# Optimization experiments

Measured on AMD Instinct MI355X. Metric: run time of the kernel, lower is better.

## Reference

```python
import jax, jax.numpy as jnp
import numpy as np

# Module hyper-params (from init_kwargs)
M = 41            # filter taps (odd)
OVERLAPS = 40     # even
STRIDES = 216
N_FFT = OVERLAPS + STRIDES   # 256
HOP = STRIDES                # strides > 0 -> hop = strides
PAD = M // 2


def setup_inputs() -> dict:
    key = jax.random.key(0)
    ks = jax.random.split(key, 5)
    B, Nmodes = 2, 2
    steps = 4628
    L = (steps - 1) * HOP + N_FFT  # 999688, frames tile the signal exactly
    x_real = jax.random.normal(ks[0], (B, L, Nmodes), jnp.float32)
    x_imag = jax.random.normal(ks[1], (B, L, Nmodes), jnp.float32)
    task_info = jax.random.uniform(ks[2], (B, 4), jnp.float32)  # col 0 = power (dBm)
    # SnseFilter learned complex taps (shared across polarizations, step=1, n_fwm=0)
    h_real = jax.random.normal(ks[3], (M,), jnp.float32) * 0.01
    h_imag = jax.random.normal(ks[4], (M,), jnp.float32) * 0.01
    return {"x_real": x_real, "x_imag": x_imag, "task_info": task_info,
            "h_real": h_real, "h_imag": h_imag}


def _corr1d(I, h):
    # I: [N, Lp] real, h: [M] real -> valid cross-correlation [N, Lp-M+1]
    out = jax.lax.conv_general_dilated(I[:, None, :], h.reshape(1, 1, M),
                                       window_strides=(1,), padding='VALID')
    return out[:, 0, :]


def reference(x_real, x_imag, task_info, h_real, h_imag):
    x = x_real + 1j * x_imag          # [B, L, Nmodes] complex64
    B, L, Nm = x.shape
    steps = (L - N_FFT) // HOP + 1

    # ---- STFT along dim=1 (frame + FFT, rectangular window, center=False) ----
    idx = HOP * jnp.arange(steps)[:, None] + jnp.arange(N_FFT)[None, :]  # [steps, n_fft]
    frames = x[:, idx, :]                      # [B, steps, n_fft, Nm]
    X = jnp.fft.fft(frames, axis=2)            # frequency-domain frames

    # ---- periodic padding along frequency axis + SnseFilter (per-tap nonlinear PBC) ----
    Xp = jnp.concatenate([X[:, :, -PAD:, :], X, X[:, :, :PAD, :]], axis=2)  # [B,steps,Lp,Nm]
    I = jnp.sum(Xp.real ** 2 + Xp.imag ** 2, axis=-1)   # total intensity over modes [B,steps,Lp]
    Lp = N_FFT + 2 * PAD
    Ic = I.reshape(B * steps, Lp)
    phi = (_corr1d(Ic, h_real) + 1j * _corr1d(Ic, h_imag)).reshape(B, steps, N_FFT)
    # launch power from task_info (col 0 in dBm), per mode
    P = (10.0 ** (task_info[:, 0] / 10.0) / Nm).astype(jnp.float32)  # [B]
    # first-order perturbation: E_out = E + j * P * (h * I) * E  (Manakov diagonal term)
    Y = X * (1.0 + 1j * P[:, None, None, None] * phi[..., None])

    # ---- ISTFT: ifft each frame + overlap-add with rectangular-window normalization ----
    yf = jnp.fft.ifft(Y, axis=2)               # [B, steps, n_fft, Nm]
    flat_idx = idx.reshape(-1)
    ola = jnp.zeros((B, L, Nm), yf.dtype).at[:, flat_idx, :].add(
        yf.reshape(B, steps * N_FFT, Nm))
    wsum = jnp.zeros((L,), jnp.float32).at[flat_idx].add(1.0)  # frame coverage count
    y = ola / wsum[None, :, None]

    out = y[:, OVERLAPS // 2: L - OVERLAPS // 2, :]   # [B, L-overlaps, Nm] complex
    return jnp.stack([out.real, out.imag], axis=-1)    # real view [B, L-overlaps, Nm, 2]
```

## Files before the change

### kernel.cpp

```cpp
#include <hip/hip_runtime.h>
#include <hip/hip_fp16.h>
#include <math.h>

constexpr int NFFT = 256;
constexpr int HOP  = 216;
constexpr int PAD  = 20;

constexpr int CBS = 264;
constexpr int IPB = 544;
constexpr int IPS = 336;
constexpr int SMF = IPB + 2 * IPS;

__device__ __forceinline__ void cmul(float& dr, float& di, float ar, float ai, float br, float bi) {
    dr = ar * br - ai * bi;
    di = ar * bi + ai * br;
}

constexpr float TC16[10] = {1.f, 0.92387953f, 0.70710678f, 0.38268343f, 0.f,
                            -0.38268343f, -0.70710678f, -0.92387953f, -1.f, -0.92387953f};
constexpr float TS16[10] = {0.f, 0.38268343f, 0.70710678f, 0.92387953f, 1.f,
                            0.92387953f, 0.70710678f, 0.38268343f, 0.f, -0.38268343f};

template<int SGN>
__device__ __forceinline__ void fft16(float xr[16], float xi[16]) {
    constexpr float S = (float)SGN;
    float tr[4][4], ti[4][4];
    #pragma unroll
    for (int n1 = 0; n1 < 4; ++n1) {
        float ar = xr[n1],      ai = xi[n1];
        float br = xr[n1 + 4],  bi = xi[n1 + 4];
        float cr = xr[n1 + 8],  ci = xi[n1 + 8];
        float dr = xr[n1 + 12], di = xi[n1 + 12];
        float Ar = ar + cr, Ai = ai + ci, Br = ar - cr, Bi = ai - ci;
        float Cr = br + dr, Ci = bi + di, Dr = br - dr, Di = bi - di;
        tr[n1][0] = Ar + Cr;      ti[n1][0] = Ai + Ci;
        tr[n1][2] = Ar - Cr;      ti[n1][2] = Ai - Ci;
        tr[n1][1] = Br - S * Di;  ti[n1][1] = Bi + S * Dr;
        tr[n1][3] = Br + S * Di;  ti[n1][3] = Bi - S * Dr;
    }
    #pragma unroll
    for (int n1 = 1; n1 < 4; ++n1) {
        #pragma unroll
        for (int k2 = 1; k2 < 4; ++k2) {
            const int m = n1 * k2;
            const float wr = TC16[m], wi = S * TS16[m];
            float vr, vi;
            cmul(vr, vi, tr[n1][k2], ti[n1][k2], wr, wi);
            tr[n1][k2] = vr; ti[n1][k2] = vi;
        }
    }
    #pragma unroll
    for (int k2 = 0; k2 < 4; ++k2) {
        float ar = tr[0][k2], ai = ti[0][k2];
        float br = tr[1][k2], bi = ti[1][k2];
        float cr = tr[2][k2], ci = ti[2][k2];
        float dr = tr[3][k2], di = ti[3][k2];
        float Ar = ar + cr, Ai = ai + ci, Br = ar - cr, Bi = ai - ci;
        float Cr = br + dr, Ci = bi + di, Dr = br - dr, Di = bi - di;
        xr[k2]      = Ar + Cr;     xi[k2]      = Ai + Ci;
        xr[k2 + 8]  = Ar - Cr;     xi[k2 + 8]  = Ai - Ci;
        xr[k2 + 4]  = Br - S * Di; xi[k2 + 4]  = Bi + S * Dr;
        xr[k2 + 12] = Br + S * Di; xi[k2 + 12] = Bi - S * Dr;
    }
}

__device__ __forceinline__ void twiddle_seq(float xr[16], float xi[16], float wr0, float wi0) {
    float wkr = wr0, wki = wi0;
    #pragma unroll
    for (int k = 1; k < 16; ++k) {
        float vr, vi;
        cmul(vr, vi, xr[k], xi[k], wkr, wki);
        xr[k] = vr; xi[k] = vi;
        if (k < 15) {
            float nr, ni;
            cmul(nr, ni, wkr, wki, wr0, wi0);
            wkr = nr; wki = ni;
        }
    }
}

__global__ __launch_bounds__(256)
void zero_overlap(float4* __restrict__ out4, int B, int steps, int Lout) {
    const int total = B * (steps - 1) * 40;
    for (int idx = blockIdx.x * 256 + threadIdx.x; idx < total; idx += gridDim.x * 256) {
        const int j  = idx / 40;
        const int r4 = idx - j * 40;
        const int b  = j / (steps - 1);
        const int s  = j - b * (steps - 1) + 1;
        out4[(size_t)b * Lout + (size_t)s * HOP - PAD + r4] = make_float4(0.f, 0.f, 0.f, 0.f);
    }
}

__global__ __launch_bounds__(64)
void eq_pbc_kernel(const float* __restrict__ x_real,
                   const float* __restrict__ x_imag,
                   const float* __restrict__ task_info,
                   const float* __restrict__ h_real,
                   const float* __restrict__ h_imag,
                   float* __restrict__ out,
                   int B, int L, int steps)
{
    __shared__ __align__(16) float SM[SMF];

    const int tid = threadIdx.x;
    const int i   = tid & 15;
    const int fm  = tid >> 4;
    const int fr  = fm >> 1;
    const int md  = fm & 1;

    const int G = B * steps;
    int g = blockIdx.x * 2 + fr;
    const bool valid = (g < G);
    if (!valid) g = G - 1;
    const int b  = g / steps;
    const int s  = g - b * steps;
    const int l0 = s * HOP;

    float sb, cb;
    __sincosf(-6.2831853071795864f * (1.0f / 256.0f) * (float)i, &sb, &cb);

    float xr[16], xi[16];
    {
        const size_t base = ((size_t)b * L + l0) * 2 + (size_t)(2 * i + md);
        #pragma unroll
        for (int n2 = 0; n2 < 16; ++n2) {
            xr[n2] = x_real[base + 32 * n2];
            xi[n2] = x_imag[base + 32 * n2];
        }
    }

    fft16<-1>(xr, xi);
    twiddle_seq(xr, xi, cb, sb);

    const int tb = fm * 272;
    #pragma unroll
    for (int k = 0; k < 16; ++k) SM[tb + i * 17 + k] = xr[k];
    __syncthreads();
    #pragma unroll
    for (int n1 = 0; n1 < 16; ++n1) xr[n1] = SM[tb + n1 * 17 + i];
    __syncthreads();
    #pragma unroll
    for (int k = 0; k < 16; ++k) SM[tb + i * 17 + k] = xi[k];
    __syncthreads();
    #pragma unroll
    for (int n1 = 0; n1 < 16; ++n1) xi[n1] = SM[tb + n1 * 17 + i];

    fft16<-1>(xr, xi);
    __syncthreads();

    {
        float* ipf = &SM[IPB + fr * IPS];
        #pragma unroll
        for (int k1 = 0; k1 < 16; ++k1) {
            float v = xr[k1] * xr[k1] + xi[k1] * xi[k1];
            v += __shfl_xor(v, 16);
            if (!md && k1 < 8) {
                const int f = i + 16 * k1, p = f + PAD;
                ipf[p + (p >> 3)] = v;
                if (f < PAD) { const int p2 = f + 276; ipf[p2 + (p2 >> 3)] = v; }
            }
            if (md && k1 >= 8) {
                const int f = i + 16 * k1, p = f + PAD;
                ipf[p + (p >> 3)] = v;
                if (f >= 236) { const int p3 = f - 236; ipf[p3 + (p3 >> 3)] = v; }
            }
        }
    }
    __syncthreads();

    {
        const int u   = tid & 31;
        const int frq = tid >> 5;
        int g2 = blockIdx.x * 2 + frq;
        if (g2 >= G) g2 = G - 1;
        const int b2 = g2 / steps;
        const float* ipb = &SM[IPB + frq * IPS + 9 * u];
        float win[8];
        #pragma unroll
        for (int j = 0; j < 8; ++j) win[j] = ipb[j + (j >> 3)];
        float phr[8], phq[8];
        #pragma unroll
        for (int o = 0; o < 8; ++o) { phr[o] = 0.f; phq[o] = 0.f; }
        #pragma unroll
        for (int t = 0; t < 41; ++t) {
            const float htr = h_real[t], hti = h_imag[t];
            #pragma unroll
            for (int o = 0; o < 8; ++o) {
                const float wv = win[(t + o) & 7];
                phr[o] = fmaf(wv, htr, phr[o]);
                phq[o] = fmaf(wv, hti, phq[o]);
            }
            if (t < 40) { const int j = t + 8; win[t & 7] = ipb[j + (j >> 3)]; }
        }
        const float P = exp2f(task_info[4 * b2] * 0.33219280948873623f) * 0.5f;
        unsigned* C = (unsigned*)SM;
        #pragma unroll
        for (int o = 0; o < 8; ++o) {
            __half2 h2 = __floats2half2_rn(1.0f - P * phq[o], P * phr[o]);
            C[frq * CBS + 8 * u + o] = *(unsigned*)&h2;
        }
    }
    __syncthreads();

    {
        const unsigned* C = (const unsigned*)SM;
        #pragma unroll
        for (int k1 = 0; k1 < 16; ++k1) {
            const unsigned cu = C[fr * CBS + i + 16 * k1];
            const __half2 h2 = *(const __half2*)&cu;
            const float cr_ = __low2float(h2);
            const float ci_ = __high2float(h2);
            const float vr = xr[k1] * cr_ - xi[k1] * ci_;
            const float vi = xr[k1] * ci_ + xi[k1] * cr_;
            xr[k1] = vr; xi[k1] = vi;
        }
    }

    fft16<1>(xr, xi);
    twiddle_seq(xr, xi, cb, -sb);
    __syncthreads();

    #pragma unroll
    for (int k = 0; k < 16; ++k) SM[tb + i * 17 + k] = xr[k];
    __syncthreads();
    #pragma unroll
    for (int k2 = 0; k2 < 16; ++k2) xr[k2] = SM[tb + k2 * 17 + i];
    __syncthreads();
    #pragma unroll
    for (int k = 0; k < 16; ++k) SM[tb + i * 17 + k] = xi[k];
    __syncthreads();
    #pragma unroll
    for (int k2 = 0; k2 < 16; ++k2) xi[k2] = SM[tb + k2 * 17 + i];

    fft16<1>(xr, xi);

    if (valid) {
        const int Lout = L - 2 * PAD;
        float* obase = out + (size_t)b * Lout * 4 + md * 2;
        #pragma unroll
        for (int n2 = 0; n2 < 16; ++n2) {
            const int n  = i + 16 * n2;
            const int la = l0 + n;
            if (la < PAD || la >= L - PAD) continue;
            const bool ov = (n < NFFT - HOP && s > 0) || (n >= HOP && s + 1 < steps);
            const float sc = (ov ? 0.5f : 1.0f) * (1.0f / 256.0f);
            float* p = obase + (size_t)(la - PAD) * 4;
            const float vr = xr[n2] * sc, vi = xi[n2] * sc;
            if (ov) { atomicAdd(p, vr); atomicAdd(p + 1, vi); }
            else    { *(float2*)p = make_float2(vr, vi); }
        }
    }
}

extern "C" void kernel_launch(void* const* d_in, const int* in_sizes, int n_in,
                              void* d_out, int out_size, void* d_ws, size_t ws_size,
                              hipStream_t stream) {
    const float* x_real    = (const float*)d_in[0];
    const float* x_imag    = (const float*)d_in[1];
    const float* task_info = (const float*)d_in[2];
    const float* h_real    = (const float*)d_in[3];
    const float* h_imag    = (const float*)d_in[4];

    const int B     = in_sizes[2] / 4;
    const int L     = in_sizes[0] / (B * 2);
    const int steps = (L - NFFT) / HOP + 1;
    const int G     = B * steps;
    const int Lout  = L - 2 * PAD;

    if (steps > 1) {
        const int total4 = B * (steps - 1) * 40;
        const int zb = (total4 + 255) / 256;
        zero_overlap<<<zb, 256, 0, stream>>>((float4*)d_out, B, steps, Lout);
    }

    eq_pbc_kernel<<<(G + 1) / 2, 64, 0, stream>>>(
        x_real, x_imag, task_info, h_real, h_imag, (float*)d_out, B, L, steps);
}
```

Measured before the change: 116.8 us.

## Replace LDS transposes with shuffle-based transpose and make waves independent

The two LDS-based 16x16 transposes in the forward and inverse FFT are replaced by a register transpose made of butterfly __shfl_xor exchanges. Each wave now owns its own LDS slice, so the __syncthreads barriers become wave-local fences. Blocks grow from 64 to 256 threads, each covering eight frames instead of two. This aims to cut LDS traffic and barrier stalls at the cost of extra shuffle and select instructions and possibly higher register pressure.

```diff
diff --git a/kernel.cpp b/kernel.cpp
--- a/kernel.cpp
+++ b/kernel.cpp
@@ -6,10 +6,10 @@
 constexpr int HOP  = 216;
 constexpr int PAD  = 20;
 
-constexpr int CBS = 264;
-constexpr int IPB = 544;
-constexpr int IPS = 336;
-constexpr int SMF = IPB + 2 * IPS;
+constexpr int IPS  = 336;
+constexpr int WSLC = 672;
+
+#define LDS_FENCE() do { asm volatile("" ::: "memory"); __builtin_amdgcn_wave_barrier(); } while (0)
 
 __device__ __forceinline__ void cmul(float& dr, float& di, float ar, float ai, float br, float bi) {
     dr = ar * br - ai * bi;
@@ -79,6 +79,25 @@
     }
 }
 
+__device__ __forceinline__ void xpose16(float r_[16], float q_[16], int i) {
+    #pragma unroll
+    for (int mi = 0; mi < 4; ++mi) {
+        const int m = 1 << mi;
+        const bool hi = (i & m) != 0;
+        #pragma unroll
+        for (int klo = 0; klo < 16; ++klo) {
+            if (klo & m) continue;
+            const int khi = klo | m;
+            float t0 = hi ? r_[klo] : r_[khi];
+            float g0 = __shfl_xor(t0, m);
+            if (hi) r_[klo] = g0; else r_[khi] = g0;
+            float t1 = hi ? q_[klo] : q_[khi];
+            float g1 = __shfl_xor(t1, m);
+            if (hi) q_[klo] = g1; else q_[khi] = g1;
+        }
+    }
+}
+
 __global__ __launch_bounds__(256)
 void zero_overlap(float4* __restrict__ out4, int B, int steps, int Lout) {
     const int total = B * (steps - 1) * 40;
@@ -91,7 +110,7 @@
     }
 }
 
-__global__ __launch_bounds__(64)
+__global__ __launch_bounds__(256)
 void eq_pbc_kernel(const float* __restrict__ x_real,
                    const float* __restrict__ x_imag,
                    const float* __restrict__ task_info,
@@ -100,16 +119,20 @@
                    float* __restrict__ out,
                    int B, int L, int steps)
 {
-    __shared__ __align__(16) float SM[SMF];
-
-    const int tid = threadIdx.x;
-    const int i   = tid & 15;
-    const int fm  = tid >> 4;
-    const int fr  = fm >> 1;
-    const int md  = fm & 1;
+    __shared__ __align__(16) float SM[4 * WSLC];
+
+    const int tid  = threadIdx.x;
+    const int wid  = tid >> 6;
+    const int lane = tid & 63;
+    const int i    = lane & 15;
+    const int fm   = lane >> 4;
+    const int fr   = fm >> 1;
+    const int md   = fm & 1;
+
+    float* wsm = SM + wid * WSLC;
 
     const int G = B * steps;
-    int g = blockIdx.x * 2 + fr;
+    int g = blockIdx.x * 8 + wid * 2 + fr;
     const bool valid = (g < G);
     if (!valid) g = G - 1;
     const int b  = g / steps;
@@ -132,24 +155,12 @@
     fft16<-1>(xr, xi);
     twiddle_seq(xr, xi, cb, sb);
 
-    const int tb = fm * 272;
-    #pragma unroll
-    for (int k = 0; k < 16; ++k) SM[tb + i * 17 + k] = xr[k];
-    __syncthreads();
-    #pragma unroll
-    for (int n1 = 0; n1 < 16; ++n1) xr[n1] = SM[tb + n1 * 17 + i];
-    __syncthreads();
-    #pragma unroll
-    for (int k = 0; k < 16; ++k) SM[tb + i * 17 + k] = xi[k];
-    __syncthreads();
-    #pragma unroll
-    for (int n1 = 0; n1 < 16; ++n1) xi[n1] = SM[tb + n1 * 17 + i];
+    xpose16(xr, xi, i);
 
     fft16<-1>(xr, xi);
-    __syncthreads();
-
-    {
-        float* ipf = &SM[IPB + fr * IPS];
+
+    {
+        float* ipf = wsm + fr * IPS;
         #pragma unroll
         for (int k1 = 0; k1 < 16; ++k1) {
             float v = xr[k1] * xr[k1] + xi[k1] * xi[k1];
@@ -166,15 +177,15 @@
             }
         }
     }
-    __syncthreads();
-
-    {
-        const int u   = tid & 31;
-        const int frq = tid >> 5;
-        int g2 = blockIdx.x * 2 + frq;
+    LDS_FENCE();
+
+    {
+        const int u   = lane & 31;
+        const int frq = lane >> 5;
+        int g2 = blockIdx.x * 8 + wid * 2 + frq;
         if (g2 >= G) g2 = G - 1;
         const int b2 = g2 / steps;
-        const float* ipb = &SM[IPB + frq * IPS + 9 * u];
+        const float* ipb = wsm + frq * IPS + 9 * u;
         float win[8];
         #pragma unroll
         for (int j = 0; j < 8; ++j) win[j] = ipb[j + (j >> 3)];
@@ -193,20 +204,22 @@
             if (t < 40) { const int j = t + 8; win[t & 7] = ipb[j + (j >> 3)]; }
         }
         const float P = exp2f(task_info[4 * b2] * 0.33219280948873623f) * 0.5f;
-        unsigned* C = (unsigned*)SM;
+        LDS_FENCE();
+        unsigned* C = (unsigned*)wsm;
         #pragma unroll
         for (int o = 0; o < 8; ++o) {
             __half2 h2 = __floats2half2_rn(1.0f - P * phq[o], P * phr[o]);
-            C[frq * CBS + 8 * u + o] = *(unsigned*)&h2;
-        }
-    }
-    __syncthreads();
-
-    {
-        const unsigned* C = (const unsigned*)SM;
+            C[frq * 288 + 9 * u + o] = *(unsigned*)&h2;
+        }
+    }
+    LDS_FENCE();
+
+    {
+        const unsigned* C = (const unsigned*)wsm;
         #pragma unroll
         for (int k1 = 0; k1 < 16; ++k1) {
-            const unsigned cu = C[fr * CBS + i + 16 * k1];
+            const int bin = i + 16 * k1;
+            const unsigned cu = C[fr * 288 + bin + (bin >> 3)];
             const __half2 h2 = *(const __half2*)&cu;
             const float cr_ = __low2float(h2);
             const float ci_ = __high2float(h2);
@@ -218,19 +231,8 @@
 
     fft16<1>(xr, xi);
     twiddle_seq(xr, xi, cb, -sb);
-    __syncthreads();
-
-    #pragma unroll
-    for (int k = 0; k < 16; ++k) SM[tb + i * 17 + k] = xr[k];
-    __syncthreads();
-    #pragma unroll
-    for (int k2 = 0; k2 < 16; ++k2) xr[k2] = SM[tb + k2 * 17 + i];
-    __syncthreads();
-    #pragma unroll
-    for (int k = 0; k < 16; ++k) SM[tb + i * 17 + k] = xi[k];
-    __syncthreads();
-    #pragma unroll
-    for (int k2 = 0; k2 < 16; ++k2) xi[k2] = SM[tb + k2 * 17 + i];
+
+    xpose16(xr, xi, i);
 
     fft16<1>(xr, xi);
 
@@ -273,6 +275,6 @@
         zero_overlap<<<zb, 256, 0, stream>>>((float4*)d_out, B, steps, Lout);
     }
 
-    eq_pbc_kernel<<<(G + 1) / 2, 64, 0, stream>>>(
+    eq_pbc_kernel<<<(G + 7) / 8, 256, 0, stream>>>(
         x_real, x_imag, task_info, h_real, h_imag, (float*)d_out, B, L, steps);
 }
```

Result: slower. 199.4 us (+70.7%).
